# Performance work log

Measured on AMD Instinct MI355X. Metric: run time of the kernel, lower is better.

## Reference

```python
import jax, jax.numpy as jnp
import numpy as np
import math

EPS = 1e-8        # numeric guard in segment intersection (matches mmcv EPSILON)
MODE_EPS = 1e-6   # module's eps
N_BOXES = 1000000


def box2corners(box):
    # box: (B, N, 5) -> corners (B, N, 4, 2)
    cx, cy, w, h, a = [box[..., i:i + 1] for i in range(5)]
    x4 = jnp.asarray([0.5, -0.5, -0.5, 0.5], box.dtype) * w   # (B,N,4)
    y4 = jnp.asarray([-0.5, -0.5, 0.5, 0.5], box.dtype) * h
    c, s = jnp.cos(a), jnp.sin(a)
    return jnp.stack([x4 * c - y4 * s + cx, x4 * s + y4 * c + cy], axis=-1)


def box_intersection(corners1, corners2):
    # all pairwise segment intersections between edges of the two boxes
    line1 = jnp.concatenate([corners1, jnp.roll(corners1, -1, axis=2)], axis=-1)  # (B,N,4,4)
    line2 = jnp.concatenate([corners2, jnp.roll(corners2, -1, axis=2)], axis=-1)
    l1 = line1[:, :, :, None, :]  # (B,N,4,1,4)
    l2 = line2[:, :, None, :, :]  # (B,N,1,4,4)
    x1, y1, x2, y2 = l1[..., 0], l1[..., 1], l1[..., 2], l1[..., 3]
    x3, y3, x4, y4 = l2[..., 0], l2[..., 1], l2[..., 2], l2[..., 3]
    num = (y4 - y3) * (x2 - x1) - (x4 - x3) * (y2 - y1)
    den_t = (x4 - x3) * (y1 - y3) - (y4 - y3) * (x1 - x3)
    t = den_t / (num + EPS)
    t_chk = jnp.where(num == 0, -1.0, t)
    mask_t = (t_chk > 0) & (t_chk < 1)
    den_u = (x2 - x1) * (y1 - y3) - (y2 - y1) * (x1 - x3)
    u = -den_u / (num + EPS)
    u_chk = jnp.where(num == 0, -1.0, u)
    mask_u = (u_chk > 0) & (u_chk < 1)
    mask = mask_t & mask_u  # (B,N,4,4)
    pts = jnp.stack([x1 + t * (x2 - x1), y1 + t * (y2 - y1)], axis=-1)
    pts = pts * mask[..., None].astype(pts.dtype)
    return pts, mask  # (B,N,4,4,2), (B,N,4,4)


def box_in_box(corners1, corners2):
    # which corners of box1 lie inside box2 (projection test)
    a = corners2[:, :, 0:1, :]
    b = corners2[:, :, 1:2, :]
    d = corners2[:, :, 3:4, :]
    ab, ad, am = b - a, d - a, corners1 - a
    p_ab = jnp.sum(ab * am, -1) / jnp.sum(ab * ab, -1)
    p_ad = jnp.sum(ad * am, -1) / jnp.sum(ad * ad, -1)
    tol = 1e-6
    return (p_ab > -tol) & (p_ab < 1 + tol) & (p_ad > -tol) & (p_ad < 1 + tol)


def intersection_area(corners1, corners2):
    # differentiable convex-intersection area via vertex sort + shoelace
    inter_pts, inter_mask = box_intersection(corners1, corners2)
    c1_in_2 = box_in_box(corners1, corners2)
    c2_in_1 = box_in_box(corners2, corners1)
    B, N = corners1.shape[:2]
    verts = jnp.concatenate([corners1, corners2, inter_pts.reshape(B, N, 16, 2)], axis=2)  # (B,N,24,2)
    mask = jnp.concatenate([c1_in_2, c2_in_1, inter_mask.reshape(B, N, 16)], axis=2)       # (B,N,24)
    num_valid = jnp.sum(mask, axis=-1, keepdims=True).astype(verts.dtype)  # (B,N,1)
    center = jnp.sum(verts * mask[..., None], axis=2) / jnp.maximum(num_valid, 1.0)  # (B,N,2)
    v = verts - center[:, :, None, :]
    ang = jnp.where(mask, jnp.arctan2(v[..., 1], v[..., 0]), 1e7)  # invalid -> end
    order = jnp.argsort(ang, axis=-1)
    v_sorted = jnp.take_along_axis(v, order[..., None], axis=2)
    m_sorted = jnp.take_along_axis(mask, order, axis=2)
    first = v_sorted[:, :, 0:1, :]
    poly = jnp.where(m_sorted[..., None], v_sorted, first)  # pad with first vertex (closes polygon)
    nxt = jnp.roll(poly, -1, axis=2)
    cross = poly[..., 0] * nxt[..., 1] - poly[..., 1] * nxt[..., 0]
    return jnp.abs(jnp.sum(cross, axis=-1)) * 0.5  # (B,N)


def diff_iou_rotated_2d(box1, box2):
    c1, c2 = box2corners(box1), box2corners(box2)
    inter = intersection_area(c1, c2)
    area1 = box1[..., 2] * box1[..., 3]
    area2 = box2[..., 2] * box2[..., 3]
    return inter / (area1 + area2 - inter)


def obb2hbb_xyxy(obb):
    cx, cy, w, h, a = obb[:, 0], obb[:, 1], obb[:, 2], obb[:, 3], obb[:, 4]
    c, s = jnp.abs(jnp.cos(a)), jnp.abs(jnp.sin(a))
    dw = (w * c + h * s) * 0.5
    dh = (w * s + h * c) * 0.5
    return jnp.stack([cx - dw, cy - dh, cx + dw, cy + dh], axis=-1)


def setup_inputs():
    key = jax.random.key(0)
    k = jax.random.split(key, 7)
    N = N_BOXES
    cxy = jax.random.uniform(k[0], (N, 2), jnp.float32, 0.0, 1024.0)
    wh = jax.random.uniform(k[1], (N, 2), jnp.float32, 8.0, 128.0)
    ang = jax.random.uniform(k[2], (N, 1), jnp.float32, -np.pi / 2, np.pi / 2)
    pred = jnp.concatenate([cxy, wh, ang], axis=-1)
    jit_xy = jax.random.uniform(k[3], (N, 2), jnp.float32, -10.0, 10.0)
    jit_wh = jax.random.uniform(k[4], (N, 2), jnp.float32, 0.8, 1.25)
    jit_a = jax.random.uniform(k[5], (N, 1), jnp.float32, -0.3, 0.3)
    target = jnp.concatenate([pred[:, :2] + jit_xy, pred[:, 2:4] * jit_wh, pred[:, 4:5] + jit_a], axis=-1)
    weight = jax.random.uniform(k[6], (N,), jnp.float32, 0.5, 1.5)
    return {"pred": pred, "target": target, "weight": weight}


def reference(pred, target, weight):
    eps = MODE_EPS
    ious = jnp.clip(diff_iou_rotated_2d(pred[None], target[None])[0], 0.0, 1.0)  # (N,)
    # enclosing HBB for penalty terms
    hp, ht = obb2hbb_xyxy(pred), obb2hbb_xyxy(target)
    en_wh = jnp.clip(jnp.maximum(hp[:, 2:], ht[:, 2:]) - jnp.minimum(hp[:, :2], ht[:, :2]), 0.0)
    c2 = en_wh[:, 0] ** 2 + en_wh[:, 1] ** 2 + eps
    rho2 = (target[:, 0] - pred[:, 0]) ** 2 + (target[:, 1] - pred[:, 1]) ** 2
    factor = 4.0 / (math.pi ** 2)
    v = factor * (jnp.arctan(target[:, 2] / (target[:, 3] + eps)) - jnp.arctan(pred[:, 2] / (pred[:, 3] + eps))) ** 2
    alpha = jax.lax.stop_gradient((ious > 0.5).astype(v.dtype) * v / (1.0 - ious + v + eps))
    cious = ious - (jnp.clip(rho2 / c2, 0.0, 1.0) + alpha * v)
    loss = (1.0 - cious) * weight
    return jnp.mean(loss)  # loss_weight=1.0, reduction='mean'
```

## Files before the change

kernel.cpp:

```cpp
#include <hip/hip_runtime.h>
#include <math.h>


#define BLOCK 256
#define NV 16

struct CEList {
    int n;
    unsigned char lo[128];
    unsigned char hi[128];
};

constexpr CEList make_ces16() {
    CEList L{};
    L.n = 0;
    for (int p = 1; p < NV; p <<= 1)
        for (int k = p; k >= 1; k >>= 1)
            for (int j = k % p; j + k < NV; j += 2 * k)
                for (int i = 0; i < k; i++) {
                    int lo = i + j, hi = i + j + k;
                    if (hi < NV && (lo / (2 * p)) == (hi / (2 * p))) {
                        L.lo[L.n] = (unsigned char)lo;
                        L.hi[L.n] = (unsigned char)hi;
                        L.n++;
                    }
                }
    return L;
}

constexpr CEList CES = make_ces16();

__device__ __forceinline__ float frcp(float x) {
    return __builtin_amdgcn_rcpf(x);
}

__device__ __forceinline__ float angle_key(float x, float y) {
    float ax = fabsf(x), ay = fabsf(y);
    float den = ax + ay;
    float r = x * frcp(den);
    r = (den > 0.f) ? r : 0.f;
    float d4 = (y >= 0.f) ? (1.f - r) : (3.f + r);
    return (d4 > 2.f) ? d4 : d4 + 4.f;
}

__device__ __forceinline__ float pair_loss(const float* __restrict__ p,
                                           const float* __restrict__ t,
                                           float wv)
{
    const float EPSf  = 1e-8f;
    const float TOLf  = 1e-6f;
    const float MEPS  = 1e-6f;
    const float PIf   = 3.14159265358979323846f;

    float pcx = p[0], pcy = p[1], pw = p[2], ph = p[3], pa = p[4];
    float tcx = t[0], tcy = t[1], tw = t[2], th = t[3], ta = t[4];

    float c1x[4], c1y[4], c2x[4], c2y[4];
    float ca = __cosf(pa), sa = __sinf(pa);
    float cb = __cosf(ta), sb = __sinf(ta);
    {
        const float xs[4] = { 0.5f, -0.5f, -0.5f, 0.5f };
        const float ys[4] = { -0.5f, -0.5f, 0.5f, 0.5f };
        #pragma unroll
        for (int k = 0; k < 4; k++) {
            float x4 = xs[k] * pw, y4 = ys[k] * ph;
            c1x[k] = x4 * ca - y4 * sa + pcx;
            c1y[k] = x4 * sa + y4 * ca + pcy;
            float x4b = xs[k] * tw, y4b = ys[k] * th;
            c2x[k] = x4b * cb - y4b * sb + tcx;
            c2y[k] = x4b * sb + y4b * cb + tcy;
        }
    }

    float vx[NV], vy[NV];
    bool  msk[NV];

    {
        float ax = c2x[0], ay = c2y[0];
        float abx = c2x[1] - ax, aby = c2y[1] - ay;
        float adx = c2x[3] - ax, ady = c2y[3] - ay;
        float rab = frcp(abx * abx + aby * aby);
        float rad = frcp(adx * adx + ady * ady);
        #pragma unroll
        for (int k = 0; k < 4; k++) {
            float amx = c1x[k] - ax, amy = c1y[k] - ay;
            float pab = (abx * amx + aby * amy) * rab;
            float pad = (adx * amx + ady * amy) * rad;
            msk[k] = (pab > -TOLf) && (pab < 1.f + TOLf) &&
                     (pad > -TOLf) && (pad < 1.f + TOLf);
            vx[k] = c1x[k]; vy[k] = c1y[k];
        }
    }
    {
        float ax = c1x[0], ay = c1y[0];
        float abx = c1x[1] - ax, aby = c1y[1] - ay;
        float adx = c1x[3] - ax, ady = c1y[3] - ay;
        float rab = frcp(abx * abx + aby * aby);
        float rad = frcp(adx * adx + ady * ady);
        #pragma unroll
        for (int k = 0; k < 4; k++) {
            float amx = c2x[k] - ax, amy = c2y[k] - ay;
            float pab = (abx * amx + aby * amy) * rab;
            float pad = (adx * amx + ady * amy) * rad;
            msk[4 + k] = (pab > -TOLf) && (pab < 1.f + TOLf) &&
                         (pad > -TOLf) && (pad < 1.f + TOLf);
            vx[4 + k] = c2x[k]; vy[4 + k] = c2y[k];
        }
    }
    #pragma unroll
    for (int e1 = 0; e1 < 4; e1++) {
        float x1 = c1x[e1], y1 = c1y[e1];
        float x2 = c1x[(e1 + 1) & 3], y2 = c1y[(e1 + 1) & 3];
        float ex = x2 - x1, ey = y2 - y1;
        float qx[4], qy[4];
        bool  qm[4];
        #pragma unroll
        for (int e2 = 0; e2 < 4; e2++) {
            float x3 = c2x[e2], y3 = c2y[e2];
            float x4 = c2x[(e2 + 1) & 3], y4 = c2y[(e2 + 1) & 3];
            float fx = x4 - x3, fy = y4 - y3;
            float num   = fy * ex - fx * ey;
            float rnum  = frcp(num + EPSf);
            float den_t = fx * (y1 - y3) - fy * (x1 - x3);
            float tt = den_t * rnum;
            float den_u = ex * (y1 - y3) - ey * (x1 - x3);
            float uu = -den_u * rnum;
            qm[e2] = (num != 0.f) && (tt > 0.f) && (tt < 1.f)
                                  && (uu > 0.f) && (uu < 1.f);
            qx[e2] = x1 + tt * ex;
            qy[e2] = y1 + tt * ey;
        }
        bool  mfL = qm[0] || qm[1];
        float fLx = qm[0] ? qx[0] : qx[1];
        float fLy = qm[0] ? qy[0] : qy[1];
        bool  msL = qm[0] && qm[1];
        bool  mfR = qm[2] || qm[3];
        float fRx = qm[2] ? qx[2] : qx[3];
        float fRy = qm[2] ? qy[2] : qy[3];
        bool  msR = qm[2] && qm[3];
        int s0 = 8 + 2 * e1, s1 = s0 + 1;
        vx[s0]  = mfL ? fLx : fRx;
        vy[s0]  = mfL ? fLy : fRy;
        msk[s0] = mfL || mfR;
        float tx = msL ? qx[1] : fRx;
        float ty = msL ? qy[1] : fRy;
        vx[s1]  = mfL ? tx : qx[3];
        vy[s1]  = mfL ? ty : qy[3];
        msk[s1] = msL || (mfL && mfR) || msR;
    }

    float sx = 0.f, sy = 0.f, cnt = 0.f;
    #pragma unroll
    for (int k = 0; k < NV; k++) {
        sx  += msk[k] ? vx[k] : 0.f;
        sy  += msk[k] ? vy[k] : 0.f;
        cnt += msk[k] ? 1.f : 0.f;
    }
    float rden = frcp(fmaxf(cnt, 1.f));
    float cxc = sx * rden, cyc = sy * rden;

    float ang[NV];
    #pragma unroll
    for (int k = 0; k < NV; k++) {
        vx[k] -= cxc;
        vy[k] -= cyc;
        ang[k] = msk[k] ? angle_key(vx[k], vy[k]) : 1e7f;
    }

    #pragma unroll
    for (int c = 0; c < CES.n; c++) {
        const int lo = CES.lo[c], hi = CES.hi[c];
        float a0 = ang[lo], a1 = ang[hi];
        bool sw = a0 > a1;
        ang[lo] = sw ? a1 : a0;  ang[hi] = sw ? a0 : a1;
        float x0 = vx[lo], x1v = vx[hi];
        vx[lo] = sw ? x1v : x0;  vx[hi] = sw ? x0 : x1v;
        float y0 = vy[lo], y1v = vy[hi];
        vy[lo] = sw ? y1v : y0;  vy[hi] = sw ? y0 : y1v;
    }

    float fx = vx[0], fy = vy[0];
    float cross = 0.f;
    #pragma unroll
    for (int k = 0; k < NV; k++) {
        int kn = (k + 1) % NV;
        bool mk = ang[k]  < 1e6f;
        bool mn = ang[kn] < 1e6f;
        float axv = mk ? vx[k]  : fx, ayv = mk ? vy[k]  : fy;
        float bxv = mn ? vx[kn] : fx, byv = mn ? vy[kn] : fy;
        cross += axv * byv - ayv * bxv;
    }
    float inter = fabsf(cross) * 0.5f;

    float area1 = pw * ph, area2 = tw * th;
    float iou = inter / (area1 + area2 - inter);
    iou = fminf(fmaxf(iou, 0.f), 1.f);

    float cA = fabsf(ca), sA = fabsf(sa);
    float cB = fabsf(cb), sB = fabsf(sb);
    float dw1 = (pw * cA + ph * sA) * 0.5f, dh1 = (pw * sA + ph * cA) * 0.5f;
    float dw2 = (tw * cB + th * sB) * 0.5f, dh2 = (tw * sB + th * cB) * 0.5f;
    float hp0 = pcx - dw1, hp1 = pcy - dh1, hp2 = pcx + dw1, hp3 = pcy + dh1;
    float ht0 = tcx - dw2, ht1 = tcy - dh2, ht2 = tcx + dw2, ht3 = tcy + dh2;

    float enw = fmaxf(fmaxf(hp2, ht2) - fminf(hp0, ht0), 0.f);
    float enh = fmaxf(fmaxf(hp3, ht3) - fminf(hp1, ht1), 0.f);
    float c2v = enw * enw + enh * enh + MEPS;
    float rho2 = (tcx - pcx) * (tcx - pcx) + (tcy - pcy) * (tcy - pcy);

    float factor = 4.f / (PIf * PIf);
    float dv = atanf(tw / (th + MEPS)) - atanf(pw / (ph + MEPS));
    float v_ = factor * dv * dv;
    float alpha = (iou > 0.5f) ? v_ / (1.f - iou + v_ + MEPS) : 0.f;

    float rhoterm = fminf(fmaxf(rho2 / c2v, 0.f), 1.f);
    float ciou = iou - (rhoterm + alpha * v_);
    return (1.f - ciou) * wv;
}

__global__ __launch_bounds__(BLOCK)
void obb_ciou_kernel(const float* __restrict__ pred,
                     const float* __restrict__ tgt,
                     const float* __restrict__ wgt,
                     float* __restrict__ out,
                     int N, float invN)
{
    int base = (blockIdx.x * blockDim.x + threadIdx.x) * 2;
    float loss = 0.f;

    #pragma unroll
    for (int u = 0; u < 2; u++) {
        int i = base + u;
        if (i < N)
            loss += pair_loss(pred + (size_t)i * 5, tgt + (size_t)i * 5,
                              wgt[i]);
    }

    #pragma unroll
    for (int off = 32; off > 0; off >>= 1)
        loss += __shfl_down(loss, off, 64);

    __shared__ float red[BLOCK / 64];
    int wave = threadIdx.x >> 6;
    int lane = threadIdx.x & 63;
    if (lane == 0) red[wave] = loss;
    __syncthreads();
    if (threadIdx.x == 0) {
        float s = 0.f;
        #pragma unroll
        for (int w = 0; w < BLOCK / 64; w++) s += red[w];
        atomicAdd(out, s * invN);
    }
}

extern "C" void kernel_launch(void* const* d_in, const int* in_sizes, int n_in,
                              void* d_out, int out_size, void* d_ws, size_t ws_size,
                              hipStream_t stream) {
    const float* pred = (const float*)d_in[0];
    const float* tgt  = (const float*)d_in[1];
    const float* wgt  = (const float*)d_in[2];
    float* out = (float*)d_out;
    int N = in_sizes[2];

    hipMemsetAsync(out, 0, sizeof(float) * (size_t)out_size, stream);

    int grid = (N + BLOCK * 2 - 1) / (BLOCK * 2);
    obb_ciou_kernel<<<grid, BLOCK, 0, stream>>>(pred, tgt, wgt, out, N,
                                                1.f / (float)N);
}
```

Baseline: 126.3 us.

## Sort packed angle-index keys and gather vertices from LDS

The bitonic network now sorts a single 32-bit key per vertex, with the angle bits packed alongside a 4-bit index, instead of swapping angle, x and y together. After sorting, the kernel gathers the centered vertices from a per-thread LDS slab, which cuts the number of selects in the sort by about a factor of three. The angle key no longer wraps into a 2..6 range, which changes the starting vertex but not the area. Each thread now handles 4 strided pairs instead of 2 adjacent ones. The 34 KB of LDS per block may limit occupancy, and truncating the low 4 bits of the angle slightly coarsens tie-breaking.

```diff
diff --git a/kernel.cpp b/kernel.cpp
--- a/kernel.cpp
+++ b/kernel.cpp
@@ -4,6 +4,8 @@
 
 #define BLOCK 256
 #define NV 16
+#define PAIRS 4
+#define LDS_STRIDE 17
 
 struct CEList {
     int n;
@@ -39,13 +41,12 @@
     float den = ax + ay;
     float r = x * frcp(den);
     r = (den > 0.f) ? r : 0.f;
-    float d4 = (y >= 0.f) ? (1.f - r) : (3.f + r);
-    return (d4 > 2.f) ? d4 : d4 + 4.f;
+    return (y >= 0.f) ? (1.f - r) : (3.f + r);
 }
 
 __device__ __forceinline__ float pair_loss(const float* __restrict__ p,
                                            const float* __restrict__ t,
-                                           float wv)
+                                           float wv, float2* __restrict__ myb)
 {
     const float EPSf  = 1e-8f;
     const float TOLf  = 1e-6f;
@@ -159,35 +160,39 @@
     float rden = frcp(fmaxf(cnt, 1.f));
     float cxc = sx * rden, cyc = sy * rden;
 
-    float ang[NV];
-    #pragma unroll
-    for (int k = 0; k < NV; k++) {
-        vx[k] -= cxc;
-        vy[k] -= cyc;
-        ang[k] = msk[k] ? angle_key(vx[k], vy[k]) : 1e7f;
+    unsigned int ku[NV];
+    #pragma unroll
+    for (int k = 0; k < NV; k++) {
+        float rx = vx[k] - cxc, ry = vy[k] - cyc;
+        myb[k] = make_float2(rx, ry);
+        float a = msk[k] ? angle_key(rx, ry) : 1e7f;
+        ku[k] = (__float_as_uint(a) & 0xFFFFFFF0u) | (unsigned int)k;
     }
 
     #pragma unroll
     for (int c = 0; c < CES.n; c++) {
         const int lo = CES.lo[c], hi = CES.hi[c];
-        float a0 = ang[lo], a1 = ang[hi];
-        bool sw = a0 > a1;
-        ang[lo] = sw ? a1 : a0;  ang[hi] = sw ? a0 : a1;
-        float x0 = vx[lo], x1v = vx[hi];
-        vx[lo] = sw ? x1v : x0;  vx[hi] = sw ? x0 : x1v;
-        float y0 = vy[lo], y1v = vy[hi];
-        vy[lo] = sw ? y1v : y0;  vy[hi] = sw ? y0 : y1v;
-    }
-
-    float fx = vx[0], fy = vy[0];
+        unsigned int a = ku[lo], b = ku[hi];
+        ku[lo] = a < b ? a : b;
+        ku[hi] = a < b ? b : a;
+    }
+
+    const unsigned int VALID_LIM = 0x49742400u;
+    float gx[NV], gy[NV];
+    bool  gv[NV];
+    #pragma unroll
+    for (int k = 0; k < NV; k++) {
+        float2 v = myb[ku[k] & 15u];
+        gx[k] = v.x; gy[k] = v.y;
+        gv[k] = ku[k] < VALID_LIM;
+    }
+    float fx = gx[0], fy = gy[0];
     float cross = 0.f;
     #pragma unroll
     for (int k = 0; k < NV; k++) {
         int kn = (k + 1) % NV;
-        bool mk = ang[k]  < 1e6f;
-        bool mn = ang[kn] < 1e6f;
-        float axv = mk ? vx[k]  : fx, ayv = mk ? vy[k]  : fy;
-        float bxv = mn ? vx[kn] : fx, byv = mn ? vy[kn] : fy;
+        float axv = gv[k]  ? gx[k]  : fx, ayv = gv[k]  ? gy[k]  : fy;
+        float bxv = gv[kn] ? gx[kn] : fx, byv = gv[kn] ? gy[kn] : fy;
         cross += axv * byv - ayv * bxv;
     }
     float inter = fabsf(cross) * 0.5f;
@@ -225,15 +230,18 @@
                      float* __restrict__ out,
                      int N, float invN)
 {
-    int base = (blockIdx.x * blockDim.x + threadIdx.x) * 2;
+    __shared__ float2 slab[BLOCK * LDS_STRIDE];
+    float2* myb = slab + (int)threadIdx.x * LDS_STRIDE;
+
+    int blk0 = blockIdx.x * (BLOCK * PAIRS);
     float loss = 0.f;
 
     #pragma unroll
-    for (int u = 0; u < 2; u++) {
-        int i = base + u;
+    for (int u = 0; u < PAIRS; u++) {
+        int i = blk0 + u * BLOCK + (int)threadIdx.x;
         if (i < N)
             loss += pair_loss(pred + (size_t)i * 5, tgt + (size_t)i * 5,
-                              wgt[i]);
+                              wgt[i], myb);
     }
 
     #pragma unroll
@@ -264,7 +272,7 @@
 
     hipMemsetAsync(out, 0, sizeof(float) * (size_t)out_size, stream);
 
-    int grid = (N + BLOCK * 2 - 1) / (BLOCK * 2);
+    int grid = (N + BLOCK * PAIRS - 1) / (BLOCK * PAIRS);
     obb_ciou_kernel<<<grid, BLOCK, 0, stream>>>(pred, tgt, wgt, out, N,
                                                 1.f / (float)N);
 }
```

Result: faster. 110.5 us (-12.5%).
